# Optimization experiments

Hardware: AMD Instinct MI355X
Metric: run time of the kernel (lower is better)

Reference implementation:

```python
import jax, jax.numpy as jnp
import numpy as np

NC = 6          # num_classes
KP = 8          # num_prototype_per_class
NPROTO = NC * KP
PH, PW = 4, 4   # patch grid (num_h, num_w)
MOM = 0.999
EPS = 1e-6


def _layernorm(x, g, b):
    mu = jnp.mean(x, axis=-1, keepdims=True)
    var = jnp.var(x, axis=-1, keepdims=True)
    return (x - mu) / jnp.sqrt(var + EPS) * g + b


def _patch_split(x, nh, nw):
    # (B,C,H,W) -> (B*nh*nw, C, H//nh, W//nw)
    B, C, H, W = x.shape
    ph, pw = H // nh, W // nw
    x = x.reshape(B, C, nh, ph, nw, pw).transpose(0, 2, 4, 1, 3, 5)
    return x.reshape(B * nh * nw, C, ph, pw)


def setup_inputs() -> dict:
    key = jax.random.key(0)
    k1, k2, k3 = jax.random.split(key, 3)
    B, C, Hh, Wh = 8, 128, 128, 128
    Horg, Worg = 512, 512
    return {
        "feats": jax.random.normal(k1, (B, C, Hh, Wh), dtype=jnp.float32),
        "gt": jax.random.randint(k2, (B, Horg, Worg), 0, 7, dtype=jnp.int64),
        "prototype": jax.random.normal(k3, (NPROTO, C), dtype=jnp.float32),
        "ln1_gamma": jnp.ones((C,), jnp.float32),
        "ln1_beta": jnp.zeros((C,), jnp.float32),
        "ln2_gamma": jnp.ones((NPROTO,), jnp.float32),
        "ln2_beta": jnp.zeros((NPROTO,), jnp.float32),
    }


def reference(feats, gt, prototype, ln1_gamma, ln1_beta, ln2_gamma, ln2_beta):
    B, C, Hh, Wh = feats.shape
    Horg, Worg = gt.shape[1], gt.shape[2]

    # --- nearest-neighbor downsample of gt to head resolution (torch 'nearest')
    ih = (jnp.arange(Hh) * Horg) // Hh
    iw = (jnp.arange(Wh) * Worg) // Wh
    label = gt[:, ih[:, None], iw[None, :]]                      # (B,Hh,Wh)
    mask = (label.astype(jnp.int32) != NC).astype(label.dtype)
    one_hot = jax.nn.one_hot(label * mask, NC, dtype=jnp.float32)  # (B,Hh,Wh,NC)
    # torch code does a raw .view(B,-1,Hh,Wh) on the contiguous one-hot; replicate
    pred0 = one_hot.reshape(B, NC, Hh, Wh)

    # --- patch split + spatial gather (softmax-weighted class centers per patch)
    pf = _patch_split(feats, PH, PW)                             # (B*16, C, ph, pw)
    pp = _patch_split(pred0, PH, PW)                             # (B*16, NC, ph, pw)
    bp = pf.shape[0]
    probs = jax.nn.softmax(pp.reshape(bp, NC, -1), axis=2)       # (B*16, NC, HWp)
    fflat = pf.reshape(bp, C, -1)                                # (B*16, C, HWp)
    ctx = jnp.einsum('bkn,bcn->bkc', probs, fflat)               # (B*16, NC, C)

    centers = ctx.reshape(B, PH * PW, NC, C)
    centers = jax.nn.gelu(_layernorm(centers, ln1_gamma, ln1_beta), approximate=False)
    centers = centers.reshape(B, PH * PW * NC, C)                # (B, 96, C)

    # --- nearest prototype assignment (cdist + argmin)
    c2 = jnp.sum(centers * centers, axis=-1)                     # (B,96)
    p2 = jnp.sum(prototype * prototype, axis=-1)                 # (48,)
    d2 = c2[:, :, None] + p2[None, None, :] - 2.0 * jnp.einsum('bmc,kc->bmk', centers, prototype)
    nearest = jnp.argmin(jnp.sqrt(jnp.maximum(d2, 0.0)), axis=-1)  # (B,96)

    # --- sequential, order-dependent momentum EMA scatter update (training path)
    sg = jax.lax.stop_gradient
    idx_flat = nearest.reshape(-1)
    ctr_flat = sg(centers.reshape(-1, C))

    def step(proto, xs):
        i, v = xs
        nv = MOM * proto[i] + (1.0 - MOM) * v
        return proto.at[i].set(nv), None

    proto_val, _ = jax.lax.scan(step, sg(prototype), (idx_flat, ctr_flat))
    # in torch the update writes .data (no grad); downstream grad w.r.t. prototype is identity
    proto_new = prototype + sg(proto_val - prototype)

    # --- prototype-to-pixel cdist similarity map
    nf = feats.reshape(B, C, -1).transpose(0, 2, 1)              # (B,HW,C)
    f2 = jnp.sum(nf * nf, axis=-1)                               # (B,HW)
    pn2 = jnp.sum(proto_new * proto_new, axis=-1)                # (48,)
    d2b = pn2[None, :, None] + f2[:, None, :] - 2.0 * jnp.einsum('kc,bnc->bkn', proto_new, nf)
    distance_l2 = jnp.sqrt(jnp.maximum(d2b, 0.0))                # (B,48,HW)

    p2c = (1.0 / (1.0 + 2.0 * distance_l2)).reshape(B, NPROTO, Hh, Wh)
    p2c = p2c.transpose(0, 2, 3, 1)
    p2c = jax.nn.gelu(_layernorm(p2c, ln2_gamma, ln2_beta), approximate=False)
    p2c_sim_map = p2c.transpose(0, 3, 1, 2)                      # (B,48,Hh,Wh)

    pred = p2c_sim_map.reshape(B, KP, NC, Hh, Wh).max(axis=1)    # (B,NC,Hh,Wh)
    pred = jax.image.resize(pred, (B, NC, Horg, Worg), method='bilinear')

    prototype_expand = jnp.broadcast_to(proto_new, (B, NPROTO, C))
    return pred, prototype_expand, p2c_sim_map, distance_l2, proto_new
```

## Files before the change

kernel.cpp:

```cpp
#include <hip/hip_runtime.h>
#include <hip/hip_bf16.h>
#include <math.h>


#define E_M1 1.71828182845904523536f
#define INV_SQRT2 0.70710678118654752440f

typedef float v2f __attribute__((ext_vector_type(2)));

__device__ __forceinline__ float gelu_exact(float x) {
    return 0.5f * x * (1.f + erff(x * INV_SQRT2));
}

__global__ __launch_bounds__(256) void kern0(const int* __restrict__ gt,
                                             unsigned char* __restrict__ labm) {
    int idx = blockIdx.x * 256 + threadIdx.x;
    int b = idx >> 14, y = (idx >> 7) & 127, x = idx & 127;
    int g = gt[(b * 512 + 4 * y) * 512 + 4 * x];
    labm[idx] = (unsigned char)((g == 6) ? 0 : g);
}

__global__ __launch_bounds__(256) void kern0b(const unsigned char* __restrict__ labm,
                                              unsigned char* __restrict__ maskb) {
    int idx = blockIdx.x * 256 + threadIdx.x;
    int b = idx >> 14, P = idx & 16383;
    const unsigned char* lm = labm + b * 16384;
    unsigned int m = 0;
    #pragma unroll
    for (int c = 0; c < 6; ++c) {
        int pos = c * 16384 + P;
        int hp = pos / 768;
        int rem = pos - hp * 768;
        int wp = rem / 6;
        int kp = rem - wp * 6;
        if ((int)lm[hp * 128 + wp] == kp) m |= (1u << c);
    }
    maskb[idx] = (unsigned char)m;
}

__global__ __launch_bounds__(128) void kernA1(
    const float* __restrict__ feats, const unsigned char* __restrict__ maskb,
    float* __restrict__ part)
{
    const int pidx = blockIdx.x;
    const int patch = pidx >> 2, q = pidx & 3;
    const int b = patch >> 4, pp = patch & 15, ihh = pp >> 2, iww = pp & 3;
    const int c = threadIdx.x;

    const float* fb = feats + (((long long)(b * 128 + c)) * 128 + ihh * 32 + q * 8) * 128 + iww * 32;
    const unsigned char* mb = maskb + b * 16384 + (ihh * 32 + q * 8) * 128 + iww * 32;

    float s0 = 0.f, s1 = 0.f, s2 = 0.f, s3 = 0.f, s4 = 0.f, s5 = 0.f, sall = 0.f;
    for (int r = 0; r < 8; ++r) {
        const float4* row = (const float4*)(fb + r * 128);
        const unsigned int* mr = (const unsigned int*)(mb + r * 128);
        #pragma unroll
        for (int j = 0; j < 8; ++j) {
            float4 v = row[j];
            unsigned int u = mr[j];
            unsigned int b0 = u, b1 = u >> 8, b2 = u >> 16, b3 = u >> 24;
            s0 += ((b0 >> 0) & 1) ? v.x : 0.f;  s1 += ((b0 >> 1) & 1) ? v.x : 0.f;
            s2 += ((b0 >> 2) & 1) ? v.x : 0.f;  s3 += ((b0 >> 3) & 1) ? v.x : 0.f;
            s4 += ((b0 >> 4) & 1) ? v.x : 0.f;  s5 += ((b0 >> 5) & 1) ? v.x : 0.f;
            s0 += ((b1 >> 0) & 1) ? v.y : 0.f;  s1 += ((b1 >> 1) & 1) ? v.y : 0.f;
            s2 += ((b1 >> 2) & 1) ? v.y : 0.f;  s3 += ((b1 >> 3) & 1) ? v.y : 0.f;
            s4 += ((b1 >> 4) & 1) ? v.y : 0.f;  s5 += ((b1 >> 5) & 1) ? v.y : 0.f;
            s0 += ((b2 >> 0) & 1) ? v.z : 0.f;  s1 += ((b2 >> 1) & 1) ? v.z : 0.f;
            s2 += ((b2 >> 2) & 1) ? v.z : 0.f;  s3 += ((b2 >> 3) & 1) ? v.z : 0.f;
            s4 += ((b2 >> 4) & 1) ? v.z : 0.f;  s5 += ((b2 >> 5) & 1) ? v.z : 0.f;
            s0 += ((b3 >> 0) & 1) ? v.w : 0.f;  s1 += ((b3 >> 1) & 1) ? v.w : 0.f;
            s2 += ((b3 >> 2) & 1) ? v.w : 0.f;  s3 += ((b3 >> 3) & 1) ? v.w : 0.f;
            s4 += ((b3 >> 4) & 1) ? v.w : 0.f;  s5 += ((b3 >> 5) & 1) ? v.w : 0.f;
            sall += v.x + v.y + v.z + v.w;
        }
    }
    float* po = part + pidx * 896;
    po[0 * 128 + c] = s0; po[1 * 128 + c] = s1; po[2 * 128 + c] = s2;
    po[3 * 128 + c] = s3; po[4 * 128 + c] = s4; po[5 * 128 + c] = s5;
    po[6 * 128 + c] = sall;
}

__global__ __launch_bounds__(512) void kernA2(
    const float* __restrict__ part, const unsigned char* __restrict__ maskb,
    const float* __restrict__ g1, const float* __restrict__ b1,
    float* __restrict__ centers, float* __restrict__ centersT)
{
    __shared__ float ct[6][128];
    __shared__ int cnt[6];

    const int tid = threadIdx.x;
    const int p = blockIdx.x;
    const int b = p >> 4, pp = p & 15, ihh = pp >> 2, iww = pp & 3;

    if (tid < 6) cnt[tid] = 0;
    __syncthreads();

    if (tid < 256) {
        const unsigned char* mb = maskb + b * 16384 + ihh * 32 * 128 + iww * 32;
        int r = tid >> 3, jw = tid & 7;
        unsigned int u = *(const unsigned int*)(mb + r * 128 + jw * 4);
        #pragma unroll
        for (int k = 0; k < 6; ++k) {
            int cc = ((u >> k) & 1) + ((u >> (8 + k)) & 1) +
                     ((u >> (16 + k)) & 1) + ((u >> (24 + k)) & 1);
            #pragma unroll
            for (int m = 1; m < 64; m <<= 1) cc += __shfl_xor(cc, m, 64);
            if ((tid & 63) == 0 && cc) atomicAdd(&cnt[k], cc);
        }
    }
    __syncthreads();

    const float* pb = part + (p * 4) * 896;
    for (int i = tid; i < 768; i += 512) {
        const int c = i & 127, k = i >> 7;
        float Sall = pb[6 * 128 + c] + pb[896 + 6 * 128 + c] +
                     pb[2 * 896 + 6 * 128 + c] + pb[3 * 896 + 6 * 128 + c];
        float Sk = pb[k * 128 + c] + pb[896 + k * 128 + c] +
                   pb[2 * 896 + k * 128 + c] + pb[3 * 896 + k * 128 + c];
        float Z = fmaf((float)cnt[k], E_M1, 1024.f);
        ct[k][c] = (Sall + E_M1 * Sk) / Z;
    }
    __syncthreads();

    const int wv = tid >> 6, lane = tid & 63;
    if (wv < 6) {
        float x0 = ct[wv][lane], x1 = ct[wv][lane + 64];
        float s = x0 + x1;
        #pragma unroll
        for (int m = 1; m < 64; m <<= 1) s += __shfl_xor(s, m, 64);
        float mu = s * (1.f / 128.f);
        float d0 = x0 - mu, d1 = x1 - mu;
        float ss = d0 * d0 + d1 * d1;
        #pragma unroll
        for (int m = 1; m < 64; m <<= 1) ss += __shfl_xor(ss, m, 64);
        float inv = 1.f / sqrtf(ss * (1.f / 128.f) + 1e-6f);
        float y0 = d0 * inv * g1[lane] + b1[lane];
        float y1 = d1 * inv * g1[lane + 64] + b1[lane + 64];
        float z0 = gelu_exact(y0);
        float z1 = gelu_exact(y1);
        const int row = (b * 16 + pp) * 6 + wv;
        centers[row * 128 + lane] = z0;
        centers[row * 128 + lane + 64] = z1;
        centersT[lane * 768 + row] = z0;
        centersT[(lane + 64) * 768 + row] = z1;
    }
}

__global__ __launch_bounds__(64) void kernC(
    const float* __restrict__ centers, const float* __restrict__ proto,
    int* __restrict__ nearest)
{
    __shared__ float cr[128];
    const int row = blockIdx.x, t = threadIdx.x;
    cr[t] = centers[row * 128 + t];
    cr[t + 64] = centers[row * 128 + 64 + t];
    __syncthreads();

    float v = INFINITY; int idx = 63;
    if (t < 48) {
        const float4* pr4 = (const float4*)(proto + t * 128);
        const float4* cr4 = (const float4*)cr;
        float d2 = 0.f;
        for (int c = 0; c < 32; ++c) {
            float4 pv = pr4[c]; float4 cv = cr4[c];
            float ax = cv.x - pv.x, ay = cv.y - pv.y, az = cv.z - pv.z, aw = cv.w - pv.w;
            d2 = fmaf(ax, ax, fmaf(ay, ay, fmaf(az, az, fmaf(aw, aw, d2))));
        }
        v = sqrtf(d2);
        idx = t;
    }
    #pragma unroll
    for (int m = 1; m < 64; m <<= 1) {
        float v2 = __shfl_xor(v, m, 64);
        int i2 = __shfl_xor(idx, m, 64);
        if (v2 < v || (v2 == v && i2 < idx)) { v = v2; idx = i2; }
    }
    if (t == 0) nearest[row] = idx;
}

__global__ __launch_bounds__(128) void kernD(
    const float* __restrict__ proto0, const int* __restrict__ nearest,
    const float* __restrict__ centersT,
    float* __restrict__ proto_new,
    float* __restrict__ out_expand, float* __restrict__ out_proto)
{
    __shared__ int nl[768];
    const int k = blockIdx.x, c = threadIdx.x;
    for (int i = c; i < 768; i += 128) nl[i] = nearest[i];
    __syncthreads();
    float p = proto0[k * 128 + c];
    const float OM = (float)(1.0 - 0.999);
    const float* col = centersT + c * 768;
    #pragma unroll 4
    for (int i = 0; i < 768; i += 4) {
        float4 v = *(const float4*)(col + i);
        if (nl[i + 0] == k) p = 0.999f * p + OM * v.x;
        if (nl[i + 1] == k) p = 0.999f * p + OM * v.y;
        if (nl[i + 2] == k) p = 0.999f * p + OM * v.z;
        if (nl[i + 3] == k) p = 0.999f * p + OM * v.w;
    }
    proto_new[k * 128 + c] = p;
    out_proto[k * 128 + c] = p;
    #pragma unroll
    for (int b = 0; b < 8; ++b) out_expand[(b * 48 + k) * 128 + c] = p;
}

__global__ __launch_bounds__(256) void kernE(
    const float* __restrict__ feats, const float* __restrict__ proto_new,
    const float* __restrict__ g2, const float* __restrict__ b2,
    float* __restrict__ out_sim, float* __restrict__ out_dist,
    float* __restrict__ pred_small)
{
    __shared__ float fT[128 * 32];
    __shared__ float prot[48 * 132];
    __shared__ float dst[32 * 49];
    __shared__ float muv[32], invv[32];

    const int t = threadIdx.x;
    const int b = blockIdx.y;
    const int nbase = blockIdx.x * 32;

    for (int i = t; i < 6144; i += 256)
        prot[(i >> 7) * 132 + (i & 127)] = proto_new[i];
    #pragma unroll
    for (int it = 0; it < 4; ++it) {
        int idx = it * 256 + t;
        int c = idx >> 3, qd = idx & 7;
        float4 v = *(const float4*)(feats + (((long long)(b * 128 + c)) << 14) + nbase + qd * 4);
        *(float4*)&fT[c * 32 + qd * 4] = v;
    }
    __syncthreads();

    const int n2 = (t & 15) * 2, k0 = (t >> 4) * 3;
    v2f acc[3];
    #pragma unroll
    for (int j = 0; j < 3; ++j) acc[j] = (v2f)(0.f);

    #pragma unroll 4
    for (int cq = 0; cq < 32; ++cq) {
        const int cb = cq * 4;
        v2f fa = *(const v2f*)&fT[(cb + 0) * 32 + n2];
        v2f fb = *(const v2f*)&fT[(cb + 1) * 32 + n2];
        v2f fc = *(const v2f*)&fT[(cb + 2) * 32 + n2];
        v2f fd = *(const v2f*)&fT[(cb + 3) * 32 + n2];
        #pragma unroll
        for (int j = 0; j < 3; ++j) {
            float4 pv = *(const float4*)&prot[(k0 + j) * 132 + cb];
            v2f t0 = fa - pv.x, t1 = fb - pv.y, t2 = fc - pv.z, t3 = fd - pv.w;
            acc[j] = __builtin_elementwise_fma(t0, t0,
                     __builtin_elementwise_fma(t1, t1,
                     __builtin_elementwise_fma(t2, t2,
                     __builtin_elementwise_fma(t3, t3, acc[j]))));
        }
    }

    #pragma unroll
    for (int j = 0; j < 3; ++j) {
        const int k = k0 + j;
        float d0 = sqrtf(acc[j].x);
        float d1 = sqrtf(acc[j].y);
        float2 dv; dv.x = d0; dv.y = d1;
        *(float2*)(out_dist + (((long long)(b * 48 + k)) << 14) + nbase + n2) = dv;
        dst[(n2 + 0) * 49 + k] = 1.f / (1.f + 2.f * d0);
        dst[(n2 + 1) * 49 + k] = 1.f / (1.f + 2.f * d1);
    }
    __syncthreads();

    if (t < 32) {
        const int n = t;
        float s = 0.f;
        for (int k = 0; k < 48; ++k) s += dst[n * 49 + k];
        float mu = s * (1.f / 48.f);
        float s2 = 0.f;
        for (int k = 0; k < 48; ++k) { float d = dst[n * 49 + k] - mu; s2 = fmaf(d, d, s2); }
        muv[n] = mu;
        invv[n] = 1.f / sqrtf(s2 * (1.f / 48.f) + 1e-6f);
    }
    __syncthreads();

    if (t < 192) {
        const int c6 = t >> 5, n = t & 31, ng = nbase + n;
        float mu = muv[n], inv = invv[n];
        float pm = 0.f;
        #pragma unroll
        for (int kp = 0; kp < 8; ++kp) {
            int k = kp * 6 + c6;
            float y = (dst[n * 49 + k] - mu) * inv * g2[k] + b2[k];
            float z = gelu_exact(y);
            out_sim[(((long long)(b * 48 + k)) << 14) + ng] = z;
            pm = (kp == 0) ? z : fmaxf(pm, z);
        }
        pred_small[((b * 6 + c6) << 14) + ng] = pm;
    }
}

__global__ __launch_bounds__(256) void kernF(
    const float* __restrict__ ps, float* __restrict__ pred)
{
    int idx = blockIdx.x * 256 + threadIdx.x;
    int xq = idx & 127;
    int oy = (idx >> 7) & 511;
    int bc = idx >> 16;
    int qy = oy >> 2, ry = oy & 3;
    int y0 = qy + ((ry < 2) ? -1 : 0);
    float fy = (ry == 0) ? 0.625f : (ry == 1) ? 0.875f : (ry == 2) ? 0.125f : 0.375f;
    int y0c = max(y0, 0), y1c = min(y0 + 1, 127);
    const float* base = ps + bc * 16384;
    const float* rA = base + y0c * 128;
    const float* rB = base + y1c * 128;
    int xm = max(xq - 1, 0), xp = min(xq + 1, 127);
    float a0 = rA[xm], a1 = rA[xq], a2 = rA[xp];
    float c0 = rB[xm], c1 = rB[xq], c2 = rB[xp];
    float w0 = 1.f - fy;
    float gm = w0 * a0 + fy * c0;
    float gc = w0 * a1 + fy * c1;
    float gp = w0 * a2 + fy * c2;
    float4 o;
    o.x = 0.375f * gm + 0.625f * gc;
    o.y = 0.125f * gm + 0.875f * gc;
    o.z = 0.875f * gc + 0.125f * gp;
    o.w = 0.625f * gc + 0.375f * gp;
    *(float4*)(pred + ((long long)idx << 2)) = o;
}

extern "C" void kernel_launch(void* const* d_in, const int* in_sizes, int n_in,
                              void* d_out, int out_size, void* d_ws, size_t ws_size,
                              hipStream_t stream)
{
    const float* feats = (const float*)d_in[0];
    const int* gt = (const int*)d_in[1];
    const float* proto = (const float*)d_in[2];
    const float* g1 = (const float*)d_in[3];
    const float* b1 = (const float*)d_in[4];
    const float* g2 = (const float*)d_in[5];
    const float* b2 = (const float*)d_in[6];

    float* out = (float*)d_out;
    float* pred       = out;
    float* out_expand = out + 12582912;
    float* out_sim    = out + 12632064;
    float* out_dist   = out + 18923520;
    float* out_proto  = out + 25214976;

    float* ws = (float*)d_ws;
    float* centers    = ws;
    float* centersT   = ws + 98304;
    float* proto_new  = ws + 196608;
    int*   nearest    = (int*)(ws + 202752);
    float* part       = ws + 203520;
    float* pred_small = ws + 203520;
    unsigned char* labm  = (unsigned char*)(ws + 989952);
    unsigned char* maskb = labm + 131072;

    kern0 <<<512, 256, 0, stream>>>(gt, labm);
    kern0b<<<512, 256, 0, stream>>>(labm, maskb);
    kernA1<<<512, 128, 0, stream>>>(feats, maskb, part);
    kernA2<<<128, 512, 0, stream>>>(part, maskb, g1, b1, centers, centersT);
    kernC <<<768, 64, 0, stream>>>(centers, proto, nearest);
    kernD <<<48, 128, 0, stream>>>(proto, nearest, centersT, proto_new,
                                   out_expand, out_proto);
    kernE <<<dim3(512, 8), 256, 0, stream>>>(feats, proto_new, g2, b2,
                                             out_sim, out_dist, pred_small);
    kernF <<<12288, 256, 0, stream>>>(pred_small, pred);
}
```

Baseline: 275.8 us.

## Fuse label/nearest kernels and use norm expansion for distance matmul

```diff
diff --git a/kernel.cpp b/kernel.cpp
--- a/kernel.cpp
+++ b/kernel.cpp
@@ -11,20 +11,13 @@
 __device__ __forceinline__ float gelu_exact(float x) {
     return 0.5f * x * (1.f + erff(x * INV_SQRT2));
 }
-
-__global__ __launch_bounds__(256) void kern0(const int* __restrict__ gt,
-                                             unsigned char* __restrict__ labm) {
-    int idx = blockIdx.x * 256 + threadIdx.x;
-    int b = idx >> 14, y = (idx >> 7) & 127, x = idx & 127;
-    int g = gt[(b * 512 + 4 * y) * 512 + 4 * x];
-    labm[idx] = (unsigned char)((g == 6) ? 0 : g);
-}
-
-__global__ __launch_bounds__(256) void kern0b(const unsigned char* __restrict__ labm,
+__device__ __forceinline__ v2f splat2(float x) { v2f r; r.x = x; r.y = x; return r; }
+
+__global__ __launch_bounds__(256) void kern0b(const int* __restrict__ gt,
                                               unsigned char* __restrict__ maskb) {
     int idx = blockIdx.x * 256 + threadIdx.x;
     int b = idx >> 14, P = idx & 16383;
-    const unsigned char* lm = labm + b * 16384;
+    const int* gb = gt + b * 262144;
     unsigned int m = 0;
     #pragma unroll
     for (int c = 0; c < 6; ++c) {
@@ -33,7 +26,9 @@
         int rem = pos - hp * 768;
         int wp = rem / 6;
         int kp = rem - wp * 6;
-        if ((int)lm[hp * 128 + wp] == kp) m |= (1u << c);
+        int g = gb[(4 * hp) * 512 + 4 * wp];
+        int lab = (g == 6) ? 0 : g;
+        if (lab == kp) m |= (1u << c);
     }
     maskb[idx] = (unsigned char)m;
 }
@@ -82,17 +77,21 @@
 
 __global__ __launch_bounds__(512) void kernA2(
     const float* __restrict__ part, const unsigned char* __restrict__ maskb,
+    const float* __restrict__ proto,
     const float* __restrict__ g1, const float* __restrict__ b1,
-    float* __restrict__ centers, float* __restrict__ centersT)
+    float* __restrict__ centersT, int* __restrict__ nearest)
 {
     __shared__ float ct[6][128];
     __shared__ int cnt[6];
+    __shared__ float pl[48 * 129];
 
     const int tid = threadIdx.x;
     const int p = blockIdx.x;
     const int b = p >> 4, pp = p & 15, ihh = pp >> 2, iww = pp & 3;
 
     if (tid < 6) cnt[tid] = 0;
+    for (int i = tid; i < 6144; i += 512)
+        pl[(i >> 7) * 129 + (i & 127)] = proto[i];
     __syncthreads();
 
     if (tid < 256) {
@@ -139,52 +138,30 @@
         float z0 = gelu_exact(y0);
         float z1 = gelu_exact(y1);
         const int row = (b * 16 + pp) * 6 + wv;
-        centers[row * 128 + lane] = z0;
-        centers[row * 128 + lane + 64] = z1;
         centersT[lane * 768 + row] = z0;
         centersT[(lane + 64) * 768 + row] = z1;
-    }
-}
-
-__global__ __launch_bounds__(64) void kernC(
-    const float* __restrict__ centers, const float* __restrict__ proto,
-    int* __restrict__ nearest)
-{
-    __shared__ float cr[128];
-    const int row = blockIdx.x, t = threadIdx.x;
-    cr[t] = centers[row * 128 + t];
-    cr[t + 64] = centers[row * 128 + 64 + t];
-    __syncthreads();
-
-    float v = INFINITY; int idx = 63;
-    if (t < 48) {
-        const float4* pr4 = (const float4*)(proto + t * 128);
-        const float4* cr4 = (const float4*)cr;
-        float d2 = 0.f;
-        for (int c = 0; c < 32; ++c) {
-            float4 pv = pr4[c]; float4 cv = cr4[c];
-            float ax = cv.x - pv.x, ay = cv.y - pv.y, az = cv.z - pv.z, aw = cv.w - pv.w;
-            d2 = fmaf(ax, ax, fmaf(ay, ay, fmaf(az, az, fmaf(aw, aw, d2))));
-        }
-        v = sqrtf(d2);
-        idx = t;
-    }
-    #pragma unroll
-    for (int m = 1; m < 64; m <<= 1) {
-        float v2 = __shfl_xor(v, m, 64);
-        int i2 = __shfl_xor(idx, m, 64);
-        if (v2 < v || (v2 == v && i2 < idx)) { v = v2; idx = i2; }
-    }
-    if (t == 0) nearest[row] = idx;
+
+        float best = INFINITY; int bi = 0;
+        for (int k = 0; k < 48; ++k) {
+            float t0 = z0 - pl[k * 129 + lane];
+            float t1 = z1 - pl[k * 129 + 64 + lane];
+            float sd = fmaf(t0, t0, t1 * t1);
+            #pragma unroll
+            for (int m = 1; m < 64; m <<= 1) sd += __shfl_xor(sd, m, 64);
+            if (sd < best) { best = sd; bi = k; }
+        }
+        if (lane == 0) nearest[row] = bi;
+    }
 }
 
 __global__ __launch_bounds__(128) void kernD(
     const float* __restrict__ proto0, const int* __restrict__ nearest,
     const float* __restrict__ centersT,
-    float* __restrict__ proto_new,
+    float* __restrict__ proto_new, float* __restrict__ pn2,
     float* __restrict__ out_expand, float* __restrict__ out_proto)
 {
     __shared__ int nl[768];
+    __shared__ float wred[2];
     const int k = blockIdx.x, c = threadIdx.x;
     for (int i = c; i < 768; i += 128) nl[i] = nearest[i];
     __syncthreads();
@@ -203,70 +180,103 @@
     out_proto[k * 128 + c] = p;
     #pragma unroll
     for (int b = 0; b < 8; ++b) out_expand[(b * 48 + k) * 128 + c] = p;
+    float sq = p * p;
+    #pragma unroll
+    for (int m = 1; m < 64; m <<= 1) sq += __shfl_xor(sq, m, 64);
+    if ((c & 63) == 0) wred[c >> 6] = sq;
+    __syncthreads();
+    if (c == 0) pn2[k] = wred[0] + wred[1];
 }
 
 __global__ __launch_bounds__(256) void kernE(
     const float* __restrict__ feats, const float* __restrict__ proto_new,
+    const float* __restrict__ pn2g,
     const float* __restrict__ g2, const float* __restrict__ b2,
     float* __restrict__ out_sim, float* __restrict__ out_dist,
     float* __restrict__ pred_small)
 {
-    __shared__ float fT[128 * 32];
+    __shared__ float fT[128 * 64];
     __shared__ float prot[48 * 132];
-    __shared__ float dst[32 * 49];
-    __shared__ float muv[32], invv[32];
+    __shared__ float p4[4 * 64];
+    __shared__ float F2[64];
+    __shared__ float muv[64], invv[64];
+    float* dst = fT;
 
     const int t = threadIdx.x;
     const int b = blockIdx.y;
-    const int nbase = blockIdx.x * 32;
+    const int nbase = blockIdx.x * 64;
 
     for (int i = t; i < 6144; i += 256)
         prot[(i >> 7) * 132 + (i & 127)] = proto_new[i];
     #pragma unroll
-    for (int it = 0; it < 4; ++it) {
+    for (int it = 0; it < 8; ++it) {
         int idx = it * 256 + t;
-        int c = idx >> 3, qd = idx & 7;
+        int c = idx >> 4, qd = idx & 15;
         float4 v = *(const float4*)(feats + (((long long)(b * 128 + c)) << 14) + nbase + qd * 4);
-        *(float4*)&fT[c * 32 + qd * 4] = v;
-    }
-    __syncthreads();
-
-    const int n2 = (t & 15) * 2, k0 = (t >> 4) * 3;
-    v2f acc[3];
-    #pragma unroll
-    for (int j = 0; j < 3; ++j) acc[j] = (v2f)(0.f);
+        *(float4*)&fT[c * 64 + qd * 4] = v;
+    }
+    __syncthreads();
+
+    {
+        int n = t & 63, cg = t >> 6;
+        float s = 0.f;
+        for (int c = cg * 32; c < cg * 32 + 32; ++c) { float x = fT[c * 64 + n]; s = fmaf(x, x, s); }
+        p4[cg * 64 + n] = s;
+    }
+    __syncthreads();
+    if (t < 64) F2[t] = ((p4[t] + p4[64 + t]) + p4[128 + t]) + p4[192 + t];
+
+    const int n4 = (t & 15) * 4, k0 = (t >> 4) * 3;
+    v2f acc[3][2];
+    #pragma unroll
+    for (int j = 0; j < 3; ++j) { acc[j][0] = splat2(0.f); acc[j][1] = splat2(0.f); }
 
     #pragma unroll 4
     for (int cq = 0; cq < 32; ++cq) {
         const int cb = cq * 4;
-        v2f fa = *(const v2f*)&fT[(cb + 0) * 32 + n2];
-        v2f fb = *(const v2f*)&fT[(cb + 1) * 32 + n2];
-        v2f fc = *(const v2f*)&fT[(cb + 2) * 32 + n2];
-        v2f fd = *(const v2f*)&fT[(cb + 3) * 32 + n2];
+        float4 f0 = *(const float4*)&fT[(cb + 0) * 64 + n4];
+        float4 f1 = *(const float4*)&fT[(cb + 1) * 64 + n4];
+        float4 f2 = *(const float4*)&fT[(cb + 2) * 64 + n4];
+        float4 f3 = *(const float4*)&fT[(cb + 3) * 64 + n4];
+        v2f f0l = *(v2f*)&f0.x, f0h = *(v2f*)&f0.z;
+        v2f f1l = *(v2f*)&f1.x, f1h = *(v2f*)&f1.z;
+        v2f f2l = *(v2f*)&f2.x, f2h = *(v2f*)&f2.z;
+        v2f f3l = *(v2f*)&f3.x, f3h = *(v2f*)&f3.z;
         #pragma unroll
         for (int j = 0; j < 3; ++j) {
             float4 pv = *(const float4*)&prot[(k0 + j) * 132 + cb];
-            v2f t0 = fa - pv.x, t1 = fb - pv.y, t2 = fc - pv.z, t3 = fd - pv.w;
-            acc[j] = __builtin_elementwise_fma(t0, t0,
-                     __builtin_elementwise_fma(t1, t1,
-                     __builtin_elementwise_fma(t2, t2,
-                     __builtin_elementwise_fma(t3, t3, acc[j]))));
-        }
-    }
-
+            v2f px = splat2(pv.x), py = splat2(pv.y), pz = splat2(pv.z), pw = splat2(pv.w);
+            acc[j][0] = __builtin_elementwise_fma(f0l, px,
+                        __builtin_elementwise_fma(f1l, py,
+                        __builtin_elementwise_fma(f2l, pz,
+                        __builtin_elementwise_fma(f3l, pw, acc[j][0]))));
+            acc[j][1] = __builtin_elementwise_fma(f0h, px,
+                        __builtin_elementwise_fma(f1h, py,
+                        __builtin_elementwise_fma(f2h, pz,
+                        __builtin_elementwise_fma(f3h, pw, acc[j][1]))));
+        }
+    }
+    __syncthreads();
+
+    float f2r0 = F2[n4 + 0], f2r1 = F2[n4 + 1], f2r2 = F2[n4 + 2], f2r3 = F2[n4 + 3];
     #pragma unroll
     for (int j = 0; j < 3; ++j) {
         const int k = k0 + j;
-        float d0 = sqrtf(acc[j].x);
-        float d1 = sqrtf(acc[j].y);
-        float2 dv; dv.x = d0; dv.y = d1;
-        *(float2*)(out_dist + (((long long)(b * 48 + k)) << 14) + nbase + n2) = dv;
-        dst[(n2 + 0) * 49 + k] = 1.f / (1.f + 2.f * d0);
-        dst[(n2 + 1) * 49 + k] = 1.f / (1.f + 2.f * d1);
-    }
-    __syncthreads();
-
-    if (t < 32) {
+        float pk = pn2g[k];
+        float d0 = sqrtf(fmaxf(f2r0 + pk - 2.f * acc[j][0].x, 0.f));
+        float d1 = sqrtf(fmaxf(f2r1 + pk - 2.f * acc[j][0].y, 0.f));
+        float d2 = sqrtf(fmaxf(f2r2 + pk - 2.f * acc[j][1].x, 0.f));
+        float d3 = sqrtf(fmaxf(f2r3 + pk - 2.f * acc[j][1].y, 0.f));
+        float4 dv; dv.x = d0; dv.y = d1; dv.z = d2; dv.w = d3;
+        *(float4*)(out_dist + (((long long)(b * 48 + k)) << 14) + nbase + n4) = dv;
+        dst[(n4 + 0) * 49 + k] = 1.f / (1.f + 2.f * d0);
+        dst[(n4 + 1) * 49 + k] = 1.f / (1.f + 2.f * d1);
+        dst[(n4 + 2) * 49 + k] = 1.f / (1.f + 2.f * d2);
+        dst[(n4 + 3) * 49 + k] = 1.f / (1.f + 2.f * d3);
+    }
+    __syncthreads();
+
+    if (t < 64) {
         const int n = t;
         float s = 0.f;
         for (int k = 0; k < 48; ++k) s += dst[n * 49 + k];
@@ -278,19 +288,23 @@
     }
     __syncthreads();
 
-    if (t < 192) {
-        const int c6 = t >> 5, n = t & 31, ng = nbase + n;
-        float mu = muv[n], inv = invv[n];
-        float pm = 0.f;
-        #pragma unroll
-        for (int kp = 0; kp < 8; ++kp) {
-            int k = kp * 6 + c6;
-            float y = (dst[n * 49 + k] - mu) * inv * g2[k] + b2[k];
-            float z = gelu_exact(y);
-            out_sim[(((long long)(b * 48 + k)) << 14) + ng] = z;
-            pm = (kp == 0) ? z : fmaxf(pm, z);
-        }
-        pred_small[((b * 6 + c6) << 14) + ng] = pm;
+    #pragma unroll
+    for (int base = 0; base < 384; base += 256) {
+        int i = base + t;
+        if (i < 384) {
+            const int c6 = i >> 6, n = i & 63, ng = nbase + n;
+            float mu = muv[n], inv = invv[n];
+            float pm = 0.f;
+            #pragma unroll
+            for (int kp = 0; kp < 8; ++kp) {
+                int k = kp * 6 + c6;
+                float y = (dst[n * 49 + k] - mu) * inv * g2[k] + b2[k];
+                float z = gelu_exact(y);
+                out_sim[(((long long)(b * 48 + k)) << 14) + ng] = z;
+                pm = (kp == 0) ? z : fmaxf(pm, z);
+            }
+            pred_small[((b * 6 + c6) << 14) + ng] = pm;
+        }
     }
 }
 
@@ -343,23 +357,20 @@
     float* out_proto  = out + 25214976;
 
     float* ws = (float*)d_ws;
-    float* centers    = ws;
     float* centersT   = ws + 98304;
     float* proto_new  = ws + 196608;
-    int*   nearest    = (int*)(ws + 202752);
-    float* part       = ws + 203520;
-    float* pred_small = ws + 203520;
-    unsigned char* labm  = (unsigned char*)(ws + 989952);
-    unsigned char* maskb = labm + 131072;
-
-    kern0 <<<512, 256, 0, stream>>>(gt, labm);
-    kern0b<<<512, 256, 0, stream>>>(labm, maskb);
+    float* pn2        = ws + 202752;
+    int*   nearest    = (int*)(ws + 202816);
+    float* part       = ws + 203584;
+    float* pred_small = ws + 203584;
+    unsigned char* maskb = (unsigned char*)(ws + 990016);
+
+    kern0b<<<512, 256, 0, stream>>>(gt, maskb);
     kernA1<<<512, 128, 0, stream>>>(feats, maskb, part);
-    kernA2<<<128, 512, 0, stream>>>(part, maskb, g1, b1, centers, centersT);
-    kernC <<<768, 64, 0, stream>>>(centers, proto, nearest);
-    kernD <<<48, 128, 0, stream>>>(proto, nearest, centersT, proto_new,
+    kernA2<<<128, 512, 0, stream>>>(part, maskb, proto, g1, b1, centersT, nearest);
+    kernD <<<48, 128, 0, stream>>>(proto, nearest, centersT, proto_new, pn2,
                                    out_expand, out_proto);
-    kernE <<<dim3(512, 8), 256, 0, stream>>>(feats, proto_new, g2, b2,
+    kernE <<<dim3(256, 8), 256, 0, stream>>>(feats, proto_new, pn2, g2, b2,
                                              out_sim, out_dist, pred_small);
     kernF <<<12288, 256, 0, stream>>>(pred_small, pred);
 }
```

Result: faster. 267.6 us (-3.0%).
